# Optimization experiments

Measured on AMD Instinct MI355X. Metric: run time of the kernel, lower is better.

Reference implementation:

```python
import jax, jax.numpy as jnp
import numpy as np

N_EMBD = 1024
HEAD_SIZE = 64


def setup_inputs() -> dict:
    key = jax.random.key(0)
    kx, kq, kk, kv = jax.random.split(key, 4)
    B, T = 8, 2048
    x = jax.random.normal(kx, (B, T, N_EMBD), dtype=jnp.float32)
    s = 1.0 / np.sqrt(N_EMBD)
    Wq = jax.random.normal(kq, (N_EMBD, HEAD_SIZE), dtype=jnp.float32) * s
    Wk = jax.random.normal(kk, (N_EMBD, HEAD_SIZE), dtype=jnp.float32) * s
    Wv = jax.random.normal(kv, (N_EMBD, HEAD_SIZE), dtype=jnp.float32) * s
    return {"x": x, "Wq": Wq, "Wk": Wk, "Wv": Wv}


def reference(x, Wq, Wk, Wv):
    # x: [B, T, C]; W*: [C, H]
    q = jnp.einsum('btc,ch->bth', x, Wq)
    k = jnp.einsum('btc,ch->bth', x, Wk)
    v = jnp.einsum('btc,ch->bth', x, Wv)
    H = q.shape[-1]
    score = jnp.einsum('bth,bsh->bts', q, k) / jnp.sqrt(jnp.asarray(H, q.dtype))
    T = score.shape[-1]
    causal = jnp.tril(jnp.ones((T, T), dtype=bool))  # [T, T]
    score = jnp.where(causal, score, -jnp.inf)
    attn = jax.nn.softmax(score, axis=-1)
    return jnp.einsum('bts,bsh->bth', attn, v)
```

## Files before the change

### kernel.cpp

```cpp
#include <hip/hip_runtime.h>

typedef __bf16 bf16;
typedef __attribute__((ext_vector_type(8))) __bf16 bf16x8;
typedef __attribute__((ext_vector_type(4))) __bf16 bf16x4;
typedef __attribute__((ext_vector_type(4))) float floatx4;

#define MFMA16(a, b, c) __builtin_amdgcn_mfma_f32_16x16x32_bf16((a), (b), (c), 0, 0, 0)

__global__ void prep_w(const float* __restrict__ Wq, const float* __restrict__ Wk,
                       const float* __restrict__ Wv, bf16* __restrict__ wTf) {
    int tid = blockIdx.x * 256 + threadIdx.x;
    int j = tid & 7;
    int l = (tid >> 3) & 15;
    int q = (tid >> 7) & 3;
    int kc = (tid >> 9) & 31;
    int mt = tid >> 14;
    int mat = mt >> 2;
    int h = ((mt & 3) << 4) + l;
    int c = kc * 32 + q * 8 + j;
    const float* W = (mat == 0) ? Wq : (mat == 1) ? Wk : Wv;
    wTf[tid] = (bf16)W[c * 64 + h];
}

#define XSTR 1032

__global__ __launch_bounds__(256, 4) void proj_qkv(const float* __restrict__ x,
                                                   const bf16* __restrict__ wTf,
                                                   bf16* __restrict__ q,
                                                   bf16* __restrict__ k,
                                                   bf16* __restrict__ vT) {
    __shared__ bf16 xs[16 * XSTR];

    const int tid = threadIdx.x;
    const int lane = tid & 63;
    const int w = tid >> 6;
    const int l15 = lane & 15;
    const int quad = lane >> 4;
    const int T0 = blockIdx.x * 16;

    {
        const int r = tid >> 4;
        const int cm = tid & 15;
        const float* g = x + (size_t)(T0 + r) * 1024 + cm * 8;
        floatx4 f[16];
        #pragma unroll
        for (int c = 0; c < 8; c++) {
            f[2 * c]     = __builtin_nontemporal_load((const floatx4*)(g + c * 128));
            f[2 * c + 1] = __builtin_nontemporal_load((const floatx4*)(g + c * 128 + 4));
        }
        bf16* ld = xs + r * XSTR + cm * 8;
        #pragma unroll
        for (int c = 0; c < 8; c++) {
            bf16x8 pk;
            pk[0] = (bf16)f[2*c][0]; pk[1] = (bf16)f[2*c][1];
            pk[2] = (bf16)f[2*c][2]; pk[3] = (bf16)f[2*c][3];
            pk[4] = (bf16)f[2*c+1][0]; pk[5] = (bf16)f[2*c+1][1];
            pk[6] = (bf16)f[2*c+1][2]; pk[7] = (bf16)f[2*c+1][3];
            *(bf16x8*)(ld + c * 128) = pk;
        }
    }
    __syncthreads();

    floatx4 acc[3] = {};
    const bf16* aw0 = wTf + (size_t)(w * 3 + 0) * 16384 + lane * 8;
    const bf16* aw1 = wTf + (size_t)(w * 3 + 1) * 16384 + lane * 8;
    const bf16* aw2 = wTf + (size_t)(w * 3 + 2) * 16384 + lane * 8;
    const bf16* xr = xs + l15 * XSTR + quad * 8;

    bf16x8 a0c = *(const bf16x8*)(aw0);
    bf16x8 a1c = *(const bf16x8*)(aw1);
    bf16x8 a2c = *(const bf16x8*)(aw2);
    bf16x8 a0n = *(const bf16x8*)(aw0 + 512);
    bf16x8 a1n = *(const bf16x8*)(aw1 + 512);
    bf16x8 a2n = *(const bf16x8*)(aw2 + 512);

    #pragma unroll 4
    for (int kc = 0; kc < 32; kc++) {
        bf16x8 p0 = *(const bf16x8*)(aw0 + (kc + 2) * 512);
        bf16x8 p1 = *(const bf16x8*)(aw1 + (kc + 2) * 512);
        bf16x8 p2 = *(const bf16x8*)(aw2 + (kc + 2) * 512);
        bf16x8 bb = *(const bf16x8*)(xr + kc * 32);
        acc[0] = MFMA16(a0c, bb, acc[0]);
        acc[1] = MFMA16(a1c, bb, acc[1]);
        acc[2] = MFMA16(a2c, bb, acc[2]);
        a0c = a0n; a1c = a1n; a2c = a2n;
        a0n = p0;  a1n = p1;  a2n = p2;
    }

    const int t = T0 + l15;
    #pragma unroll
    for (int i = 0; i < 3; i++) {
        int mtile = w * 3 + i;
        int mat = mtile >> 2;
        int hbase = ((mtile & 3) << 4) + (quad << 2);
        float sc = (mat == 0) ? 0.125f : 1.0f;
        bf16x4 pk;
        pk[0] = (bf16)(acc[i][0] * sc);
        pk[1] = (bf16)(acc[i][1] * sc);
        pk[2] = (bf16)(acc[i][2] * sc);
        pk[3] = (bf16)(acc[i][3] * sc);
        if (mat == 0) {
            *(bf16x4*)(q + (size_t)t * 64 + hbase) = pk;
        } else if (mat == 1) {
            *(bf16x4*)(k + (size_t)t * 64 + hbase) = pk;
        } else {
            int b = t >> 11, tt = t & 2047;
            #pragma unroll
            for (int r = 0; r < 4; r++)
                vT[(size_t)(b * 64 + hbase + r) * 2048 + tt] = pk[r];
        }
    }
}

#define KP2 72
#define OH 68

__global__ __launch_bounds__(512, 4) void flash(const bf16* __restrict__ q,
                                                const bf16* __restrict__ k,
                                                const bf16* __restrict__ vT,
                                                float* __restrict__ out) {
    __shared__ char smem[8 * 16 * OH * 4];
    __shared__ float Ms[8][16], Ls[8][16];
    bf16* psall = (bf16*)smem;
    float* Os = (float*)smem;

    const int b = blockIdx.x & 7;
    const int p = blockIdx.x >> 3;
    const int t0A = p * 16;
    const int t0B = (127 - p) * 16;
    const int nttA = (p >> 2) + 1;
    const int nttB = ((127 - p) >> 2) + 1;
    const int L = nttA + nttB;

    const int tid = threadIdx.x;
    const int w = tid >> 6;
    const int lane = tid & 63;
    const int l15 = lane & 15;
    const int quad = lane >> 4;

    const int s0 = (L * w) >> 3;
    const int s1 = (L * (w + 1)) >> 3;

    const bf16* kbase = k + (size_t)(b * 2048 + l15) * 64 + quad * 8;
    const bf16* vbase = vT + (size_t)(b * 64 + l15) * 2048 + quad * 8;
    bf16* psw = psall + w * 16 * KP2;

    const bf16* qpA = q + (size_t)(b * 2048 + t0A + l15) * 64 + quad * 8;
    const bf16* qpB = q + (size_t)(b * 2048 + t0B + l15) * 64 + quad * 8;
    bf16x8 qfA0 = *(const bf16x8*)qpA;
    bf16x8 qfA1 = *(const bf16x8*)(qpA + 32);
    bf16x8 qfB0 = *(const bf16x8*)qpB;
    bf16x8 qfB1 = *(const bf16x8*)(qpB + 32);

    floatx4 oA[4] = {}, oB[4] = {};
    float miA = -1e30f, liA = 0.f, miB = -1e30f, liB = 0.f;

    bf16x8 kf[8];
    {
        int j0 = (s0 < nttA) ? s0 : (s0 - nttA);
        const bf16* kp = kbase + (size_t)j0 * 4096;
        #pragma unroll
        for (int mt = 0; mt < 4; mt++) {
            kf[2 * mt]     = *(const bf16x8*)(kp + mt * 1024);
            kf[2 * mt + 1] = *(const bf16x8*)(kp + mt * 1024 + 32);
        }
    }

#define KV_STEP(sv, jtv, isdiag, t0v, qf0v, qf1v, mi_, li_, o_)                      \
    {                                                                                 \
        floatx4 stt[4];                                                               \
        _Pragma("unroll") for (int mt = 0; mt < 4; mt++) {                            \
            floatx4 z = {};                                                           \
            z = MFMA16(kf[2 * mt], qf0v, z);                                          \
            z = MFMA16(kf[2 * mt + 1], qf1v, z);                                      \
            stt[mt] = z;                                                              \
        }                                                                             \
        {                 \
            int snx = (sv) + 1;                                                       \
            if (snx < s1) {                                                           \
                int jn = (snx < nttA) ? snx : (snx - nttA);                           \
                const bf16* kpn = kbase + (size_t)jn * 4096;                          \
                _Pragma("unroll") for (int mt = 0; mt < 4; mt++) {                    \
                    kf[2 * mt]     = *(const bf16x8*)(kpn + mt * 1024);               \
                    kf[2 * mt + 1] = *(const bf16x8*)(kpn + mt * 1024 + 32);          \
                }                                                                     \
            }                                                                         \
        }                                                                             \
        if (isdiag) {                                                                 \
            _Pragma("unroll") for (int mt = 0; mt < 4; mt++)                          \
                _Pragma("unroll") for (int r = 0; r < 4; r++) {                       \
                    int kv = (jtv) * 64 + mt * 16 + quad * 4 + r;                     \
                    if (kv > (t0v) + l15) stt[mt][r] = -1e30f;                        \
                }                                                                     \
        }                                                                             \
        float mx = fmaxf(fmaxf(fmaxf(stt[0][0], stt[0][1]), fmaxf(stt[0][2], stt[0][3])),  \
                         fmaxf(fmaxf(stt[1][0], stt[1][1]), fmaxf(stt[1][2], stt[1][3]))); \
        mx = fmaxf(mx, fmaxf(fmaxf(fmaxf(stt[2][0], stt[2][1]), fmaxf(stt[2][2], stt[2][3])),  \
                             fmaxf(fmaxf(stt[3][0], stt[3][1]), fmaxf(stt[3][2], stt[3][3])))); \
        mx = fmaxf(mx, __shfl_xor(mx, 16, 64));                                       \
        mx = fmaxf(mx, __shfl_xor(mx, 32, 64));                                       \
        float mnew = fmaxf(mi_, mx);                                                  \
        float aa = __expf(mi_ - mnew);                                                \
        mi_ = mnew;                                                                   \
        float rs = 0.f;                                                               \
        _Pragma("unroll") for (int mt = 0; mt < 4; mt++)                              \
            _Pragma("unroll") for (int r = 0; r < 4; r++) {                           \
                float pv = __expf(stt[mt][r] - mnew);                                 \
                stt[mt][r] = pv;                                                      \
                rs += pv;                                                             \
            }                                                                         \
        rs += __shfl_xor(rs, 16, 64);                                                 \
        rs += __shfl_xor(rs, 32, 64);                                                 \
        li_ = li_ * aa + rs;                                                          \
        _Pragma("unroll") for (int mt = 0; mt < 4; mt++)                              \
            _Pragma("unroll") for (int r = 0; r < 4; r++) o_[mt][r] *= aa;            \
        _Pragma("unroll") for (int mt = 0; mt < 4; mt++) {                            \
            bf16x4 pk;                                                                \
            pk[0] = (bf16)stt[mt][0]; pk[1] = (bf16)stt[mt][1];                       \
            pk[2] = (bf16)stt[mt][2]; pk[3] = (bf16)stt[mt][3];                       \
            *(bf16x4*)(psw + l15 * KP2 + mt * 16 + quad * 4) = pk;                    \
        }                                                                             \
        const bf16* vp = vbase + (jtv) * 64;                                          \
        _Pragma("unroll") for (int kc = 0; kc < 2; kc++) {                            \
            bf16x8 pb = *(const bf16x8*)(psw + l15 * KP2 + kc * 32 + quad * 8);       \
            _Pragma("unroll") for (int mt = 0; mt < 4; mt++) {                        \
                bf16x8 va = *(const bf16x8*)(vp + mt * 32768 + kc * 32);              \
                o_[mt] = MFMA16(va, pb, o_[mt]);                                      \
            }                                                                         \
        }                                                                             \
    }

    {
        const int eA = (s1 < nttA) ? s1 : nttA;
        for (int s = s0; s < eA; s++) {
            KV_STEP(s, s, (s == nttA - 1), t0A, qfA0, qfA1, miA, liA, oA);
        }
    }
    {
        const int sB = (s0 > nttA) ? s0 : nttA;
        for (int s = sB; s < s1; s++) {
            KV_STEP(s, s - nttA, (s == L - 1), t0B, qfB0, qfB1, miB, liB, oB);
        }
    }
#undef KV_STEP

    #pragma unroll
    for (int tile = 0; tile < 2; tile++) {
        __syncthreads();
        float mi = tile ? miB : miA;
        float li = tile ? liB : liA;
        if (lane < 16) { Ms[w][lane] = mi; Ls[w][lane] = li; }
        #pragma unroll
        for (int mt = 0; mt < 4; mt++) {
            floatx4 ov = tile ? oB[mt] : oA[mt];
            *(floatx4*)(Os + (w * 16 + l15) * OH + mt * 16 + quad * 4) = ov;
        }
        __syncthreads();
        {
            int qq = tid >> 5;
            int h2 = (tid & 31) * 2;
            float Mg = -1e30f;
            #pragma unroll
            for (int u = 0; u < 8; u++) Mg = fmaxf(Mg, Ms[u][qq]);
            float Lg = 0.f, v0 = 0.f, v1 = 0.f;
            #pragma unroll
            for (int u = 0; u < 8; u++) {
                float sw = __expf(Ms[u][qq] - Mg);
                Lg += sw * Ls[u][qq];
                const float* Or = Os + (u * 16 + qq) * OH + h2;
                v0 += sw * Or[0];
                v1 += sw * Or[1];
            }
            float inv = 1.0f / Lg;
            int t0v = tile ? t0B : t0A;
            float* op = out + (size_t)(b * 2048 + t0v + qq) * 64 + h2;
            __builtin_nontemporal_store(v0 * inv, op);
            __builtin_nontemporal_store(v1 * inv, op + 1);
        }
    }
}

extern "C" void kernel_launch(void* const* d_in, const int* in_sizes, int n_in,
                              void* d_out, int out_size, void* d_ws, size_t ws_size,
                              hipStream_t stream) {
    const float* x  = (const float*)d_in[0];
    const float* Wq = (const float*)d_in[1];
    const float* Wk = (const float*)d_in[2];
    const float* Wv = (const float*)d_in[3];
    float* out = (float*)d_out;

    char* ws = (char*)d_ws;
    bf16* wTf = (bf16*)ws;
    bf16* q   = (bf16*)(ws + 397312);
    bf16* k   = (bf16*)(ws + 397312 + 2097152);
    bf16* vT  = (bf16*)(ws + 397312 + 2 * 2097152);

    hipLaunchKernelGGL(prep_w,   dim3(768),  dim3(256), 0, stream, Wq, Wk, Wv, wTf);
    hipLaunchKernelGGL(proj_qkv, dim3(1024), dim3(256), 0, stream, x, wTf, q, k, vT);
    hipLaunchKernelGGL(flash,    dim3(512),  dim3(512), 0, stream, q, k, vT, out);
}
```

Measured before the change: 153.7 us.

## Double token tile in projection with swizzled LDS; widen flash to 16 waves with tree merge

The projection kernel now handles 32 tokens per block and uses an XOR-swizzled LDS layout in place of padding. Each weight fragment feeds two MFMAs, which halves weight reloads per token, and weight prefetch now runs three steps ahead. The flash kernel grows to 1024 threads (16 waves), splitting the KV range more finely, and replaces the one-shot 8-way merge with a log-depth pairwise reduction through LDS. The cost is more __syncthreads rounds, higher register pressure from the larger accumulator tile, and half as many projection blocks.

```diff
diff --git a/kernel.cpp b/kernel.cpp
--- a/kernel.cpp
+++ b/kernel.cpp
@@ -22,107 +22,123 @@
     wTf[tid] = (bf16)W[c * 64 + h];
 }
 
-#define XSTR 1032
-
 __global__ __launch_bounds__(256, 4) void proj_qkv(const float* __restrict__ x,
                                                    const bf16* __restrict__ wTf,
                                                    bf16* __restrict__ q,
                                                    bf16* __restrict__ k,
                                                    bf16* __restrict__ vT) {
-    __shared__ bf16 xs[16 * XSTR];
+    __shared__ bf16 xs[32 * 1024];
 
     const int tid = threadIdx.x;
     const int lane = tid & 63;
     const int w = tid >> 6;
     const int l15 = lane & 15;
     const int quad = lane >> 4;
-    const int T0 = blockIdx.x * 16;
+    const int T0 = blockIdx.x * 32;
 
     {
-        const int r = tid >> 4;
-        const int cm = tid & 15;
+        const int r = tid >> 3;
+        const int cm = tid & 7;
         const float* g = x + (size_t)(T0 + r) * 1024 + cm * 8;
-        floatx4 f[16];
-        #pragma unroll
-        for (int c = 0; c < 8; c++) {
-            f[2 * c]     = __builtin_nontemporal_load((const floatx4*)(g + c * 128));
-            f[2 * c + 1] = __builtin_nontemporal_load((const floatx4*)(g + c * 128 + 4));
-        }
-        bf16* ld = xs + r * XSTR + cm * 8;
-        #pragma unroll
-        for (int c = 0; c < 8; c++) {
-            bf16x8 pk;
-            pk[0] = (bf16)f[2*c][0]; pk[1] = (bf16)f[2*c][1];
-            pk[2] = (bf16)f[2*c][2]; pk[3] = (bf16)f[2*c][3];
-            pk[4] = (bf16)f[2*c+1][0]; pk[5] = (bf16)f[2*c+1][1];
-            pk[6] = (bf16)f[2*c+1][2]; pk[7] = (bf16)f[2*c+1][3];
-            *(bf16x8*)(ld + c * 128) = pk;
+        bf16* ld = xs + r * 1024;
+        const int sw = r & 7;
+        #pragma unroll
+        for (int jb = 0; jb < 4; jb++) {
+            floatx4 f[8];
+            #pragma unroll
+            for (int jj = 0; jj < 4; jj++) {
+                f[2*jj]   = __builtin_nontemporal_load((const floatx4*)(g + (jb*4+jj) * 64));
+                f[2*jj+1] = __builtin_nontemporal_load((const floatx4*)(g + (jb*4+jj) * 64 + 4));
+            }
+            #pragma unroll
+            for (int jj = 0; jj < 4; jj++) {
+                int gg = cm + (jb*4+jj) * 8;
+                bf16x8 pk;
+                pk[0] = (bf16)f[2*jj][0]; pk[1] = (bf16)f[2*jj][1];
+                pk[2] = (bf16)f[2*jj][2]; pk[3] = (bf16)f[2*jj][3];
+                pk[4] = (bf16)f[2*jj+1][0]; pk[5] = (bf16)f[2*jj+1][1];
+                pk[6] = (bf16)f[2*jj+1][2]; pk[7] = (bf16)f[2*jj+1][3];
+                *(bf16x8*)(ld + ((gg ^ sw) << 3)) = pk;
+            }
         }
     }
     __syncthreads();
 
-    floatx4 acc[3] = {};
+    floatx4 acc[3][2] = {};
     const bf16* aw0 = wTf + (size_t)(w * 3 + 0) * 16384 + lane * 8;
     const bf16* aw1 = wTf + (size_t)(w * 3 + 1) * 16384 + lane * 8;
     const bf16* aw2 = wTf + (size_t)(w * 3 + 2) * 16384 + lane * 8;
-    const bf16* xr = xs + l15 * XSTR + quad * 8;
-
-    bf16x8 a0c = *(const bf16x8*)(aw0);
-    bf16x8 a1c = *(const bf16x8*)(aw1);
-    bf16x8 a2c = *(const bf16x8*)(aw2);
-    bf16x8 a0n = *(const bf16x8*)(aw0 + 512);
-    bf16x8 a1n = *(const bf16x8*)(aw1 + 512);
-    bf16x8 a2n = *(const bf16x8*)(aw2 + 512);
-
-    #pragma unroll 4
+    const bf16* xr0 = xs + l15 * 1024;
+    const bf16* xr1 = xs + (16 + l15) * 1024;
+    const int swz = l15 & 7;
+
+    bf16x8 A0[3], A1[3], A2[3];
+    #pragma unroll
+    for (int i = 0; i < 3; i++) {
+        A0[i] = *(const bf16x8*)(aw0 + i * 512);
+        A1[i] = *(const bf16x8*)(aw1 + i * 512);
+        A2[i] = *(const bf16x8*)(aw2 + i * 512);
+    }
+
+    #pragma unroll
     for (int kc = 0; kc < 32; kc++) {
-        bf16x8 p0 = *(const bf16x8*)(aw0 + (kc + 2) * 512);
-        bf16x8 p1 = *(const bf16x8*)(aw1 + (kc + 2) * 512);
-        bf16x8 p2 = *(const bf16x8*)(aw2 + (kc + 2) * 512);
-        bf16x8 bb = *(const bf16x8*)(xr + kc * 32);
-        acc[0] = MFMA16(a0c, bb, acc[0]);
-        acc[1] = MFMA16(a1c, bb, acc[1]);
-        acc[2] = MFMA16(a2c, bb, acc[2]);
-        a0c = a0n; a1c = a1n; a2c = a2n;
-        a0n = p0;  a1n = p1;  a2n = p2;
-    }
-
-    const int t = T0 + l15;
+        const int idx = kc % 3;
+        bf16x8 a0 = A0[idx], a1 = A1[idx], a2 = A2[idx];
+        if (kc < 29) {
+            A0[idx] = *(const bf16x8*)(aw0 + (kc + 3) * 512);
+            A1[idx] = *(const bf16x8*)(aw1 + (kc + 3) * 512);
+            A2[idx] = *(const bf16x8*)(aw2 + (kc + 3) * 512);
+        }
+        const int sl = (((kc * 4 + quad) ^ swz) << 3);
+        bf16x8 b0 = *(const bf16x8*)(xr0 + sl);
+        bf16x8 b1 = *(const bf16x8*)(xr1 + sl);
+        acc[0][0] = MFMA16(a0, b0, acc[0][0]);
+        acc[0][1] = MFMA16(a0, b1, acc[0][1]);
+        acc[1][0] = MFMA16(a1, b0, acc[1][0]);
+        acc[1][1] = MFMA16(a1, b1, acc[1][1]);
+        acc[2][0] = MFMA16(a2, b0, acc[2][0]);
+        acc[2][1] = MFMA16(a2, b1, acc[2][1]);
+    }
+
     #pragma unroll
     for (int i = 0; i < 3; i++) {
         int mtile = w * 3 + i;
         int mat = mtile >> 2;
         int hbase = ((mtile & 3) << 4) + (quad << 2);
         float sc = (mat == 0) ? 0.125f : 1.0f;
-        bf16x4 pk;
-        pk[0] = (bf16)(acc[i][0] * sc);
-        pk[1] = (bf16)(acc[i][1] * sc);
-        pk[2] = (bf16)(acc[i][2] * sc);
-        pk[3] = (bf16)(acc[i][3] * sc);
-        if (mat == 0) {
-            *(bf16x4*)(q + (size_t)t * 64 + hbase) = pk;
-        } else if (mat == 1) {
-            *(bf16x4*)(k + (size_t)t * 64 + hbase) = pk;
-        } else {
-            int b = t >> 11, tt = t & 2047;
-            #pragma unroll
-            for (int r = 0; r < 4; r++)
-                vT[(size_t)(b * 64 + hbase + r) * 2048 + tt] = pk[r];
+        #pragma unroll
+        for (int tt = 0; tt < 2; tt++) {
+            int t = T0 + tt * 16 + l15;
+            bf16x4 pk;
+            pk[0] = (bf16)(acc[i][tt][0] * sc);
+            pk[1] = (bf16)(acc[i][tt][1] * sc);
+            pk[2] = (bf16)(acc[i][tt][2] * sc);
+            pk[3] = (bf16)(acc[i][tt][3] * sc);
+            if (mat == 0) {
+                *(bf16x4*)(q + (size_t)t * 64 + hbase) = pk;
+            } else if (mat == 1) {
+                *(bf16x4*)(k + (size_t)t * 64 + hbase) = pk;
+            } else {
+                int b = t >> 11, tts = t & 2047;
+                #pragma unroll
+                for (int r = 0; r < 4; r++)
+                    vT[(size_t)(b * 64 + hbase + r) * 2048 + tts] = pk[r];
+            }
         }
     }
 }
 
 #define KP2 72
-#define OH 68
-
-__global__ __launch_bounds__(512, 4) void flash(const bf16* __restrict__ q,
-                                                const bf16* __restrict__ k,
-                                                const bf16* __restrict__ vT,
-                                                float* __restrict__ out) {
-    __shared__ char smem[8 * 16 * OH * 4];
-    __shared__ float Ms[8][16], Ls[8][16];
+#define OH2 68
+
+__global__ __launch_bounds__(1024, 4) void flash(const bf16* __restrict__ q,
+                                                 const bf16* __restrict__ k,
+                                                 const bf16* __restrict__ vT,
+                                                 float* __restrict__ out) {
+    __shared__ char smem[16 * 16 * KP2 * 2];
+    __shared__ float Mb[8][16], Lb[8][16];
     bf16* psall = (bf16*)smem;
-    float* Os = (float*)smem;
+    float* Ob = (float*)smem;
 
     const int b = blockIdx.x & 7;
     const int p = blockIdx.x >> 3;
@@ -138,8 +154,8 @@
     const int l15 = lane & 15;
     const int quad = lane >> 4;
 
-    const int s0 = (L * w) >> 3;
-    const int s1 = (L * (w + 1)) >> 3;
+    const int s0 = (L * w) >> 4;
+    const int s1 = (L * (w + 1)) >> 4;
 
     const bf16* kbase = k + (size_t)(b * 2048 + l15) * 64 + quad * 8;
     const bf16* vbase = vT + (size_t)(b * 64 + l15) * 2048 + quad * 8;
@@ -232,50 +248,76 @@
 
     {
         const int eA = (s1 < nttA) ? s1 : nttA;
-        for (int s = s0; s < eA; s++) {
+        for (int s = s0; s < eA; s++)
             KV_STEP(s, s, (s == nttA - 1), t0A, qfA0, qfA1, miA, liA, oA);
-        }
     }
     {
         const int sB = (s0 > nttA) ? s0 : nttA;
-        for (int s = sB; s < s1; s++) {
+        for (int s = sB; s < s1; s++)
             KV_STEP(s, s - nttA, (s == L - 1), t0B, qfB0, qfB1, miB, liB, oB);
-        }
     }
 #undef KV_STEP
 
-    #pragma unroll
-    for (int tile = 0; tile < 2; tile++) {
-        __syncthreads();
-        float mi = tile ? miB : miA;
-        float li = tile ? liB : liA;
-        if (lane < 16) { Ms[w][lane] = mi; Ls[w][lane] = li; }
+#define MERGE_ROUND(act, mi_, li_, o_)                                                \
+    {                                                                                 \
+        const int half = (act) >> 1;                                                  \
+        __syncthreads();                                                              \
+        if (w >= half && w < (act)) {                                                 \
+            if (lane < 16) { Mb[w - half][lane] = mi_; Lb[w - half][lane] = li_; }    \
+            _Pragma("unroll") for (int mt = 0; mt < 4; mt++)                          \
+                *(floatx4*)(Ob + ((w - half) * 16 + l15) * OH2 + mt * 16 + quad * 4) = o_[mt]; \
+        }                                                                             \
+        __syncthreads();                                                              \
+        if (w < half) {                                                               \
+            float m2 = Mb[w][l15], l2 = Lb[w][l15];                                   \
+            float Mn = fmaxf(mi_, m2);                                                \
+            float a1 = __expf(mi_ - Mn), a2 = __expf(m2 - Mn);                        \
+            mi_ = Mn;                                                                 \
+            li_ = li_ * a1 + l2 * a2;                                                 \
+            _Pragma("unroll") for (int mt = 0; mt < 4; mt++) {                        \
+                floatx4 o2 = *(const floatx4*)(Ob + (w * 16 + l15) * OH2 + mt * 16 + quad * 4); \
+                o_[mt] = o_[mt] * a1 + o2 * a2;                                       \
+            }                                                                         \
+        }                                                                             \
+    }
+
+    MERGE_ROUND(16, miA, liA, oA)
+    MERGE_ROUND(8,  miA, liA, oA)
+    MERGE_ROUND(4,  miA, liA, oA)
+    MERGE_ROUND(2,  miA, liA, oA)
+    MERGE_ROUND(16, miB, liB, oB)
+    MERGE_ROUND(8,  miB, liB, oB)
+    MERGE_ROUND(4,  miB, liB, oB)
+#undef MERGE_ROUND
+
+    __syncthreads();
+    if (w == 0) {
+        if (lane < 16) { Mb[0][lane] = miB; Lb[0][lane] = liB; }
+        #pragma unroll
+        for (int mt = 0; mt < 4; mt++)
+            *(floatx4*)(Ob + l15 * OH2 + mt * 16 + quad * 4) = oB[mt];
+    }
+    __syncthreads();
+    if (w == 1) {
+        float m2 = Mb[0][l15], l2 = Lb[0][l15];
+        float Mn = fmaxf(miB, m2);
+        float a1 = __expf(miB - Mn), a2 = __expf(m2 - Mn);
+        float Lg = liB * a1 + l2 * a2;
+        float inv = 1.0f / Lg;
+        float* op = out + (size_t)(b * 2048 + t0B + l15) * 64;
         #pragma unroll
         for (int mt = 0; mt < 4; mt++) {
-            floatx4 ov = tile ? oB[mt] : oA[mt];
-            *(floatx4*)(Os + (w * 16 + l15) * OH + mt * 16 + quad * 4) = ov;
-        }
-        __syncthreads();
-        {
-            int qq = tid >> 5;
-            int h2 = (tid & 31) * 2;
-            float Mg = -1e30f;
-            #pragma unroll
-            for (int u = 0; u < 8; u++) Mg = fmaxf(Mg, Ms[u][qq]);
-            float Lg = 0.f, v0 = 0.f, v1 = 0.f;
-            #pragma unroll
-            for (int u = 0; u < 8; u++) {
-                float sw = __expf(Ms[u][qq] - Mg);
-                Lg += sw * Ls[u][qq];
-                const float* Or = Os + (u * 16 + qq) * OH + h2;
-                v0 += sw * Or[0];
-                v1 += sw * Or[1];
-            }
-            float inv = 1.0f / Lg;
-            int t0v = tile ? t0B : t0A;
-            float* op = out + (size_t)(b * 2048 + t0v + qq) * 64 + h2;
-            __builtin_nontemporal_store(v0 * inv, op);
-            __builtin_nontemporal_store(v1 * inv, op + 1);
+            floatx4 o2 = *(const floatx4*)(Ob + l15 * OH2 + mt * 16 + quad * 4);
+            floatx4 ov = (oB[mt] * a1 + o2 * a2) * inv;
+            *(floatx4*)(op + mt * 16 + quad * 4) = ov;
+        }
+    } else if (w == 0) {
+        float inv = 1.0f / liA;
+        float* op = out + (size_t)(b * 2048 + t0A + l15) * 64;
+        #pragma unroll
+        for (int mt = 0; mt < 4; mt++) {
+            floatx4 ov = oA[mt] * inv;
+            *(floatx4*)(op + mt * 16 + quad * 4) = ov;
         }
     }
 }
@@ -295,7 +337,7 @@
     bf16* k   = (bf16*)(ws + 397312 + 2097152);
     bf16* vT  = (bf16*)(ws + 397312 + 2 * 2097152);
 
-    hipLaunchKernelGGL(prep_w,   dim3(768),  dim3(256), 0, stream, Wq, Wk, Wv, wTf);
-    hipLaunchKernelGGL(proj_qkv, dim3(1024), dim3(256), 0, stream, x, wTf, q, k, vT);
-    hipLaunchKernelGGL(flash,    dim3(512),  dim3(512), 0, stream, q, k, vT, out);
+    hipLaunchKernelGGL(prep_w,   dim3(768), dim3(256),  0, stream, Wq, Wk, Wv, wTf);
+    hipLaunchKernelGGL(proj_qkv, dim3(512), dim3(256),  0, stream, x, wTf, q, k, vT);
+    hipLaunchKernelGGL(flash,    dim3(512), dim3(1024), 0, stream, q, k, vT, out);
 }
```

New measurement: 160.0 us. 4.1% more time.
